# Performance work log

Hardware: AMD Instinct MI355X
Metric: run time of the kernel (lower is better)

The kernel has to match this reference:

```python
import jax, jax.numpy as jnp
import numpy as np

D = 1024      # feature_dim / vertice_dim
H = 4         # n_heads
HD = D // H   # head dim 256
DFF = 2 * D   # 2048
DV = 1024     # vertice_dim
T = 64        # frame_num
PERIOD = 30
NEG = -1e9


def setup_inputs() -> dict:
    key = jax.random.key(0)
    ks = iter(jax.random.split(key, 32))
    sc = 0.02
    def w(shape):
        return jax.random.normal(next(ks), shape, dtype=jnp.float32) * sc
    return {
        "hidden_states": jax.random.normal(next(ks), (T, DV), dtype=jnp.float32),
        "hid_w": w((D, DV)), "hid_b": w((D,)),
        "obj_w": w((D, 80)),
        "sa_in_w": w((3 * D, D)), "sa_in_b": w((3 * D,)),
        "sa_out_w": w((D, D)), "sa_out_b": w((D,)),
        "ca_in_w": w((3 * D, D)), "ca_in_b": w((3 * D,)),
        "ca_out_w": w((D, D)), "ca_out_b": w((D,)),
        "ln1_g": jnp.ones((D,), jnp.float32), "ln1_b": jnp.zeros((D,), jnp.float32),
        "ln2_g": jnp.ones((D,), jnp.float32), "ln2_b": jnp.zeros((D,), jnp.float32),
        "ln3_g": jnp.ones((D,), jnp.float32), "ln3_b": jnp.zeros((D,), jnp.float32),
        "ff1_w": w((DFF, D)), "ff1_b": w((DFF,)),
        "ff2_w": w((D, DFF)), "ff2_b": w((D,)),
        "vr_w": w((DV, D)), "vr_b": w((DV,)),
        "vm_w": w((D, DV)), "vm_b": w((D,)),
    }


def _periodic_pe():
    # sin/cos PE over one period, tiled (PeriodicPositionalEncoding)
    pos = jnp.arange(PERIOD, dtype=jnp.float32)[:, None]
    div = jnp.exp(jnp.arange(0, D, 2, dtype=jnp.float32) * (-np.log(10000.0) / D))
    pe = jnp.zeros((PERIOD, D), jnp.float32)
    pe = pe.at[:, 0::2].set(jnp.sin(pos * div)).at[:, 1::2].set(jnp.cos(pos * div))
    reps = T // PERIOD + 1
    return jnp.tile(pe, (reps, 1))[:T]  # (T, D)


def reference(hidden_states, hid_w, hid_b, obj_w,
              sa_in_w, sa_in_b, sa_out_w, sa_out_b,
              ca_in_w, ca_in_b, ca_out_w, ca_out_b,
              ln1_g, ln1_b, ln2_g, ln2_b, ln3_g, ln3_b,
              ff1_w, ff1_b, ff2_w, ff2_b, vr_w, vr_b, vm_w, vm_b):
    mem = hidden_states @ hid_w.T + hid_b          # (S=T, D)
    style = obj_w[:, 0]                             # one-hot(0) @ obj_vector
    pe = _periodic_pe()

    # ALiBi-style biased causal mask (init_biased_mask, n_head=4)
    slopes = 0.25 ** jnp.arange(1, H + 1, dtype=jnp.float32)
    idx = jnp.arange(T)
    i_, j_ = idx[:, None], idx[None, :]
    alibi = -((i_ - j_) // PERIOD).astype(jnp.float32)
    tgt_bias = jnp.where(j_ <= i_, slopes[:, None, None] * alibi[None], NEG)  # (H,T,T)
    # vocaset enc_dec_mask: frame i may only attend memory frame i
    mem_bias = jnp.where(i_ == j_, 0.0, NEG)  # (T,S)

    def mha(q_in, kv_in, in_w, in_b, out_w, out_b, bias):
        wq, wk, wv = jnp.split(in_w, 3, axis=0)
        bq, bk, bv = jnp.split(in_b, 3)
        q = (q_in @ wq.T + bq).reshape(-1, H, HD)
        k = (kv_in @ wk.T + bk).reshape(-1, H, HD)
        v = (kv_in @ wv.T + bv).reshape(-1, H, HD)
        s = jnp.einsum('qhd,khd->hqk', q, k) / np.sqrt(HD) + bias
        a = jax.nn.softmax(s, axis=-1)
        o = jnp.einsum('hqk,khd->qhd', a, v).reshape(-1, D)
        return o @ out_w.T + out_b

    def ln(x, g, b):
        m = x.mean(-1, keepdims=True)
        v = ((x - m) ** 2).mean(-1, keepdims=True)
        return (x - m) / jnp.sqrt(v + 1e-5) * g + b

    def decode(x):  # post-norm TransformerDecoderLayer (eval, dropout off)
        x = ln(x + mha(x, x, sa_in_w, sa_in_b, sa_out_w, sa_out_b, tgt_bias), ln1_g, ln1_b)
        x = ln(x + mha(x, mem, ca_in_w, ca_in_b, ca_out_w, ca_out_b, mem_bias[None]), ln2_g, ln2_b)
        h = jax.nn.relu(x @ ff1_w.T + ff1_b) @ ff2_w.T + ff2_b
        return ln(x + h, ln3_g, ln3_b)

    # independent of the zero-padded future slots, matching the growing-seq loop.
    emb0 = jnp.zeros((T, D), jnp.float32).at[0].set(style)

    def step(emb, i):
        out = decode(emb + pe)
        new_tok = (out[i] @ vr_w.T + vr_b) @ vm_w.T + vm_b + style
        return emb.at[i + 1].set(new_tok), None

    emb, _ = jax.lax.scan(step, emb0, jnp.arange(T - 1))
    # final iteration's vertice_out over the full T-length sequence
    return decode(emb + pe) @ vr_w.T + vr_b  # (T, DV)
```

## Files before the change

### kernel.cpp

```cpp
#include <hip/hip_runtime.h>
#include <math.h>

#define DIM  1024
#define SEQ  64
#define HDIM 256
#define NBLK 256

__device__ __forceinline__ float wsum(float v){
  v += __shfl_xor(v, 32, 64); v += __shfl_xor(v, 16, 64); v += __shfl_xor(v, 8, 64);
  v += __shfl_xor(v, 4, 64);  v += __shfl_xor(v, 2, 64);  v += __shfl_xor(v, 1, 64);
  return v;
}
__device__ __forceinline__ float wmax(float v){
  v = fmaxf(v, __shfl_xor(v, 32, 64)); v = fmaxf(v, __shfl_xor(v, 16, 64));
  v = fmaxf(v, __shfl_xor(v, 8, 64));  v = fmaxf(v, __shfl_xor(v, 4, 64));
  v = fmaxf(v, __shfl_xor(v, 2, 64));  v = fmaxf(v, __shfl_xor(v, 1, 64));
  return v;
}
__device__ __forceinline__ float2 breduce2(float va, float vb, float* red){
  int tid = threadIdx.x;
  va = wsum(va); vb = wsum(vb);
  if ((tid & 63) == 0){ red[(tid >> 6) * 2] = va; red[(tid >> 6) * 2 + 1] = vb; }
  __syncthreads();
  float ra = red[0] + red[2] + red[4] + red[6];
  float rb = red[1] + red[3] + red[5] + red[7];
  __syncthreads();
  return make_float2(ra, rb);
}

__device__ __forceinline__ float ldc(const float* p){
  return __hip_atomic_load(p, __ATOMIC_RELAXED, __HIP_MEMORY_SCOPE_AGENT);
}
__device__ __forceinline__ void stc(float* p, float v){
  __hip_atomic_store(p, v, __ATOMIC_RELAXED, __HIP_MEMORY_SCOPE_AGENT);
}

__device__ __forceinline__ void spin_ge(unsigned* p, unsigned ep){
  unsigned spins = 0;
  while (__hip_atomic_load(p, __ATOMIC_RELAXED, __HIP_MEMORY_SCOPE_AGENT) < ep){
    if (++spins > 4194304u){
      unsigned s2 = 0;
      while (__hip_atomic_load(p, __ATOMIC_ACQUIRE, __HIP_MEMORY_SCOPE_AGENT) < ep){
        __builtin_amdgcn_s_sleep(2);
        if (++s2 > 100000000u) break;
      }
      return;
    }
  }
}

#define SLOT_STRIDE 32
__device__ __forceinline__ void gsync(unsigned* slots, unsigned ep, int bid, int tid){
  asm volatile("s_waitcnt vmcnt(0)" ::: "memory");
  __syncthreads();
  if (tid == 0)
    __hip_atomic_store(&slots[bid * SLOT_STRIDE], ep, __ATOMIC_RELAXED, __HIP_MEMORY_SCOPE_AGENT);
  spin_ge(&slots[tid * SLOT_STRIDE], ep);
  __syncthreads();
  asm volatile("" ::: "memory");
}

__global__ void matmul_nn_1024(const float* __restrict__ A, const float* __restrict__ B,
                               float* __restrict__ Cc){
  __shared__ float As[32][33];
  __shared__ float Bs[32][33];
  int tb = blockIdx.x * 32, ta = blockIdx.y * 32;
  int tx = threadIdx.x & 31, ty = threadIdx.x >> 5;
  float acc[4] = {0.f, 0.f, 0.f, 0.f};
  for (int k0 = 0; k0 < 1024; k0 += 32){
    for (int r = ty; r < 32; r += 8) As[r][tx] = A[(size_t)(ta + r) * 1024 + k0 + tx];
    for (int r = ty; r < 32; r += 8) Bs[r][tx] = B[(size_t)(k0 + r) * 1024 + tb + tx];
    __syncthreads();
    #pragma unroll
    for (int kk = 0; kk < 32; ++kk){
      float bv = Bs[kk][tx];
      #pragma unroll
      for (int m = 0; m < 4; ++m) acc[m] = fmaf(As[ty + 8 * m][kk], bv, acc[m]);
    }
    __syncthreads();
  }
  for (int m = 0; m < 4; ++m) Cc[(size_t)(ta + ty + 8 * m) * 1024 + tb + tx] = acc[m];
}

struct CoopArgs {
  const float *hs, *hid_w, *hid_b;
  const float *sa_in_w, *sa_in_b, *sa_out_w, *sa_out_b;
  const float *ca_in_w, *ca_in_b, *ca_out_w, *ca_out_b;
  const float *ln1_g, *ln1_b, *ln2_g, *ln2_b, *ln3_g, *ln3_b;
  const float *ff1_w, *ff1_b, *ff2_w, *ff2_b;
  const float *vr_w, *vr_b, *vm_w, *vm_b, *obj_w;
  const float *Cm;
  float *pe, *emb, *kc, *vc, *mem, *vtmp, *cac, *q, *u, *hb, *w, *s;
  float *out;
  unsigned *bar;
  unsigned *flags;
};

__global__ void __launch_bounds__(256, 2) decode_loop(CoopArgs a){
  const int tid = threadIdx.x, bid = blockIdx.x;
  const int wave = tid >> 6, lane = tid & 63;
  const int gw = bid * 4 + wave;
  __shared__ float sm[2048];
  __shared__ float scp[256];
  __shared__ float red[8];
  unsigned* slots = a.bar;
  unsigned ep = 0;

  const float NLOG = -9.210340371976184f / 1024.0f;
  const float divw = __expf((float)(2 * (gw >> 1)) * NLOG);
  const int parw = gw & 1;

  {
    float pw[16];
    const float* pr = a.hid_w + (size_t)gw * DIM;
    #pragma unroll
    for (int k = 0; k < 16; ++k) pw[k] = pr[lane + 64 * k];
    float bias = a.hid_b[gw];
    for (int t = 0; t < 64; ++t){
      const float* xr = a.hs + (size_t)t * DIM;
      float acc = 0.f;
      #pragma unroll
      for (int k = 0; k < 16; ++k) acc = fmaf(pw[k], xr[lane + 64 * k], acc);
      acc = wsum(acc);
      if (lane == 0) stc(a.mem + (size_t)t * DIM + gw, acc + bias);
    }
    {
      float arg = (float)(lane % 30) * divw;
      float pev = parw ? cosf(arg) : sinf(arg);
      stc(a.pe + (size_t)lane * DIM + gw, pev);
    }
    if (bid == 0){
      for (int d = tid; d < DIM; d += 256) stc(a.emb + d, a.obj_w[(size_t)d * 80]);
    }
  }
  ++ep; gsync(slots, ep, bid, tid);

  {
    float pw[16];
    const float* pr = a.ca_in_w + (size_t)(2 * DIM + gw) * DIM;
    #pragma unroll
    for (int k = 0; k < 16; ++k) pw[k] = pr[lane + 64 * k];
    float bias = a.ca_in_b[2 * DIM + gw];
    for (int t = 0; t < 64; ++t){
      const float* xr = a.mem + (size_t)t * DIM;
      #pragma unroll
      for (int k = 0; k < 4; ++k) sm[tid + 256 * k] = ldc(xr + tid + 256 * k);
      __syncthreads();
      float acc = 0.f;
      #pragma unroll
      for (int k = 0; k < 16; ++k) acc = fmaf(pw[k], sm[lane + 64 * k], acc);
      acc = wsum(acc);
      if (lane == 0) stc(a.vtmp + (size_t)t * DIM + gw, acc + bias);
      __syncthreads();
    }
  }
  ++ep; gsync(slots, ep, bid, tid);

  {
    float pw[16];
    const float* pr = a.ca_out_w + (size_t)gw * DIM;
    #pragma unroll
    for (int k = 0; k < 16; ++k) pw[k] = pr[lane + 64 * k];
    float bias = a.ca_out_b[gw];
    for (int t = 0; t < 64; ++t){
      const float* xr = a.vtmp + (size_t)t * DIM;
      #pragma unroll
      for (int k = 0; k < 4; ++k) sm[tid + 256 * k] = ldc(xr + tid + 256 * k);
      __syncthreads();
      float acc = 0.f;
      #pragma unroll
      for (int k = 0; k < 16; ++k) acc = fmaf(pw[k], sm[lane + 64 * k], acc);
      acc = wsum(acc);
      if (lane == 0) stc(a.cac + (size_t)t * DIM + gw, acc + bias);
      __syncthreads();
    }
  }
  ++ep; gsync(slots, ep, bid, tid);

  float wq[16], wk[16], wv[16], wo[16], f1a[16], f1b[16], f2[32];
  {
    const float* pq = a.sa_in_w + (size_t)gw * DIM;
    const float* pk = a.sa_in_w + (size_t)(DIM + gw) * DIM;
    const float* pv = a.sa_in_w + (size_t)(2 * DIM + gw) * DIM;
    const float* po = a.sa_out_w + (size_t)gw * DIM;
    const float* p1a = a.ff1_w + (size_t)(2 * gw) * DIM;
    const float* p1b = a.ff1_w + (size_t)(2 * gw + 1) * DIM;
    const float* p2 = a.ff2_w + (size_t)gw * 2048;
    #pragma unroll
    for (int k = 0; k < 16; ++k){
      int d = lane + 64 * k;
      wq[k] = pq[d]; wk[k] = pk[d]; wv[k] = pv[d]; wo[k] = po[d];
      f1a[k] = p1a[d]; f1b[k] = p1b[d];
    }
    #pragma unroll
    for (int k = 0; k < 32; ++k) f2[k] = p2[lane + 64 * k];
  }
  const float b_q  = a.sa_in_b[gw];
  const float b_k  = a.sa_in_b[DIM + gw];
  const float b_v  = a.sa_in_b[2 * DIM + gw];
  const float b_o  = a.sa_out_b[gw];
  const float b_1a = a.ff1_b[2 * gw];
  const float b_1b = a.ff1_b[2 * gw + 1];
  const float b_2  = a.ff2_b[gw];
  const float b_vr = a.vr_b[gw];
  float cbv;
  {
    const float* pv = a.vm_w + (size_t)gw * DIM;
    float acc = 0.f;
    #pragma unroll
    for (int k = 0; k < 16; ++k) acc = fmaf(pv[lane + 64 * k], a.vr_b[lane + 64 * k], acc);
    cbv = wsum(acc) + a.vm_b[gw] + a.obj_w[(size_t)gw * 80];
  }

  float c0 = 0.f, c1 = 0.f, c2 = 0.f, c3 = 0.f;

  const bool is_score = (bid < 16);
  const int sc_h  = bid >> 2;
  const int sc_jg = bid & 3;
  const float sc_slope = 1.0f / (float)(4 << (2 * sc_h));

  for (int i = 0; i < SEQ; ++i){
    const float* per = a.pe + (size_t)i * DIM;

    {
      float* xs = sm;
      const float* er = a.emb + (size_t)i * DIM;
      #pragma unroll
      for (int k = 0; k < 4; ++k){
        int d = tid + 256 * k;
        xs[d] = ldc(er + d) + ldc(per + d);
      }
      __syncthreads();
      float aq = 0.f, ak = 0.f, av = 0.f;
      #pragma unroll
      for (int k = 0; k < 16; ++k){
        float x = xs[lane + 64 * k];
        aq = fmaf(wq[k], x, aq);
        ak = fmaf(wk[k], x, ak);
        av = fmaf(wv[k], x, av);
      }
      aq = wsum(aq); ak = wsum(ak); av = wsum(av);
      if (lane == 0){
        stc(a.q + gw, aq + b_q);
        stc(a.kc + (size_t)i * DIM + gw, ak + b_k);
        stc(a.vc + (size_t)i * DIM + gw, av + b_v);
      }
      __syncthreads();
    }
    ++ep; gsync(slots, ep, bid, tid);

    {
      float* xs  = sm;
      float* qsl = sm + 1024;
      float remb = ldc(a.emb + (size_t)i * DIM + gw);
      #pragma unroll
      for (int k = 0; k < 4; ++k) xs[tid + 256 * k] = ldc(a.vc + (size_t)i * DIM + tid + 256 * k);
      if (is_score) qsl[tid] = ldc(a.q + sc_h * HDIM + tid);
      __syncthreads();
      float p0 = 0.f, p1 = 0.f, p2 = 0.f, p3 = 0.f;
      #pragma unroll
      for (int k = 0; k < 4; ++k){
        p0 = fmaf(wo[k],      xs[lane + 64 * k],        p0);
        p1 = fmaf(wo[k + 4],  xs[lane + 64 * (k + 4)],  p1);
        p2 = fmaf(wo[k + 8],  xs[lane + 64 * (k + 8)],  p2);
        p3 = fmaf(wo[k + 12], xs[lane + 64 * (k + 12)], p3);
      }
      p0 = wsum(p0); p1 = wsum(p1); p2 = wsum(p2); p3 = wsum(p3);
      if (lane == i){ c0 = p0; c1 = p1; c2 = p2; c3 = p3; }
      if (is_score){
        #pragma unroll
        for (int jj = 0; jj < 4; ++jj){
          int j = sc_jg * 16 + wave * 4 + jj;
          if (j <= i){
            const float* kr = a.kc + (size_t)j * DIM + sc_h * HDIM;
            float acc = 0.f;
            #pragma unroll
            for (int m = 0; m < 4; ++m)
              acc = fmaf(qsl[m * 64 + lane], ldc(kr + m * 64 + lane), acc);
            acc = wsum(acc);
            if (lane == 0)
              stc(a.s + sc_h * 64 + j, acc * 0.0625f - sc_slope * (float)((i - j) / 30));
          }
        }
        asm volatile("s_waitcnt vmcnt(0)" ::: "memory");
        __syncthreads();
        if (tid == 0)
          __hip_atomic_store(&a.flags[bid * SLOT_STRIDE], (unsigned)(i + 1),
                             __ATOMIC_RELAXED, __HIP_MEMORY_SCOPE_AGENT);
      }
      if (tid < 16) spin_ge(&a.flags[tid * SLOT_STRIDE], (unsigned)(i + 1));
      __syncthreads();
      {
        const int h = wave;
        float sv = (lane <= i) ? ldc(a.s + h * 64 + lane) : -3.0e38f;
        float mx = wmax(sv);
        float p = (lane <= i) ? __expf(sv - mx) : 0.f;
        float sum = wsum(p);
        scp[h * 64 + lane] = p / sum;
      }
      __syncthreads();
      float t = scp[lane] * c0 + scp[64 + lane] * c1 + scp[128 + lane] * c2 + scp[192 + lane] * c3;
      t = wsum(t);
      if (lane == 0){
        stc(a.u + gw, remb + ldc(per + gw) + t + b_o);
      }
      __syncthreads();
    }
    ++ep; gsync(slots, ep, bid, tid);

    float x2v;
    {
      float* xs = sm;
      #pragma unroll
      for (int k = 0; k < 4; ++k) xs[tid + 256 * k] = ldc(a.u + tid + 256 * k);
      __syncthreads();
      float sa = 0.f, sb = 0.f;
      #pragma unroll
      for (int k = 0; k < 4; ++k){ float x = xs[tid + 256 * k]; sa += x; sb = fmaf(x, x, sb); }
      float2 r = breduce2(sa, sb, red);
      float mean = r.x * (1.f / 1024.f);
      float var = r.y * (1.f / 1024.f) - mean * mean;
      float rs = 1.f / sqrtf(var + 1e-5f);
      float tv[4];
      float ta = 0.f, tb = 0.f;
      #pragma unroll
      for (int k = 0; k < 4; ++k){
        int d = tid + 256 * k;
        float x1 = (xs[d] - mean) * rs * a.ln1_g[d] + a.ln1_b[d];
        tv[k] = x1 + ldc(a.cac + (size_t)i * DIM + d);
        ta += tv[k]; tb = fmaf(tv[k], tv[k], tb);
      }
      float2 r2 = breduce2(ta, tb, red);
      float mean2 = r2.x * (1.f / 1024.f);
      float var2 = r2.y * (1.f / 1024.f) - mean2 * mean2;
      float rs2 = 1.f / sqrtf(var2 + 1e-5f);
      #pragma unroll
      for (int k = 0; k < 4; ++k){
        int d = tid + 256 * k;
        xs[d] = (tv[k] - mean2) * rs2 * a.ln2_g[d] + a.ln2_b[d];
      }
      __syncthreads();
      x2v = xs[gw];
      float acc0 = 0.f, acc1 = 0.f;
      #pragma unroll
      for (int k = 0; k < 16; ++k){
        float x = xs[lane + 64 * k];
        acc0 = fmaf(f1a[k], x, acc0);
        acc1 = fmaf(f1b[k], x, acc1);
      }
      acc0 = wsum(acc0); acc1 = wsum(acc1);
      if (lane == 0){
        stc(a.hb + 2 * gw,     fmaxf(acc0 + b_1a, 0.f));
        stc(a.hb + 2 * gw + 1, fmaxf(acc1 + b_1b, 0.f));
      }
      __syncthreads();
    }
    ++ep; gsync(slots, ep, bid, tid);

    float vrr[16], cmr[16];
    {
      float* hsm = sm;
      #pragma unroll
      for (int k = 0; k < 8; ++k) hsm[tid + 256 * k] = ldc(a.hb + tid + 256 * k);
      const float* pr = a.vr_w + (size_t)gw * DIM;
      const float* pc = a.Cm + (size_t)gw * DIM;
      #pragma unroll
      for (int k = 0; k < 16; ++k){ vrr[k] = pr[lane + 64 * k]; cmr[k] = pc[lane + 64 * k]; }
      __syncthreads();
      float acc = 0.f;
      #pragma unroll
      for (int k = 0; k < 32; ++k) acc = fmaf(f2[k], hsm[lane + 64 * k], acc);
      acc = wsum(acc);
      if (lane == 0) stc(a.w + gw, x2v + acc + b_2);
      __syncthreads();
    }
    ++ep; gsync(slots, ep, bid, tid);

    {
      float* xs = sm;
      #pragma unroll
      for (int k = 0; k < 4; ++k) xs[tid + 256 * k] = ldc(a.w + tid + 256 * k);
      __syncthreads();
      float sa = 0.f, sb = 0.f;
      #pragma unroll
      for (int k = 0; k < 4; ++k){ float x = xs[tid + 256 * k]; sa += x; sb = fmaf(x, x, sb); }
      float2 r = breduce2(sa, sb, red);
      float mean = r.x * (1.f / 1024.f);
      float var = r.y * (1.f / 1024.f) - mean * mean;
      float rs = 1.f / sqrtf(var + 1e-5f);
      float ov[4];
      #pragma unroll
      for (int k = 0; k < 4; ++k){
        int d = tid + 256 * k;
        ov[k] = (xs[d] - mean) * rs * a.ln3_g[d] + a.ln3_b[d];
      }
      __syncthreads();
      #pragma unroll
      for (int k = 0; k < 4; ++k) xs[tid + 256 * k] = ov[k];
      __syncthreads();
      {
        float ar = 0.f, ac = 0.f;
        #pragma unroll
        for (int k = 0; k < 16; ++k){
          float x = xs[lane + 64 * k];
          ar = fmaf(vrr[k], x, ar);
          ac = fmaf(cmr[k], x, ac);
        }
        ar = wsum(ar); ac = wsum(ac);
        if (lane == 0){
          a.out[(size_t)i * DIM + gw] = ar + b_vr;
          if (i < SEQ - 1) stc(a.emb + (size_t)(i + 1) * DIM + gw, ac + cbv);
        }
      }
      __syncthreads();
    }
    ++ep; gsync(slots, ep, bid, tid);
  }
}

extern "C" void kernel_launch(void* const* d_in, const int* in_sizes, int n_in,
                              void* d_out, int out_size, void* d_ws, size_t ws_size,
                              hipStream_t stream){
  const float* hs       = (const float*)d_in[0];
  const float* hid_w    = (const float*)d_in[1];
  const float* hid_b    = (const float*)d_in[2];
  const float* obj_w    = (const float*)d_in[3];
  const float* sa_in_w  = (const float*)d_in[4];
  const float* sa_in_b  = (const float*)d_in[5];
  const float* sa_out_w = (const float*)d_in[6];
  const float* sa_out_b = (const float*)d_in[7];
  const float* ca_in_w  = (const float*)d_in[8];
  const float* ca_in_b  = (const float*)d_in[9];
  const float* ca_out_w = (const float*)d_in[10];
  const float* ca_out_b = (const float*)d_in[11];
  const float* ln1_g    = (const float*)d_in[12];
  const float* ln1_b    = (const float*)d_in[13];
  const float* ln2_g    = (const float*)d_in[14];
  const float* ln2_b    = (const float*)d_in[15];
  const float* ln3_g    = (const float*)d_in[16];
  const float* ln3_b    = (const float*)d_in[17];
  const float* ff1_w    = (const float*)d_in[18];
  const float* ff1_b    = (const float*)d_in[19];
  const float* ff2_w    = (const float*)d_in[20];
  const float* ff2_b    = (const float*)d_in[21];
  const float* vr_w     = (const float*)d_in[22];
  const float* vr_b     = (const float*)d_in[23];
  const float* vm_w     = (const float*)d_in[24];
  const float* vm_b     = (const float*)d_in[25];

  float* ws = (float*)d_ws;
  float* pe   = ws;
  float* emb  = ws + 65536;
  float* kc   = ws + 131072;
  float* vc   = ws + 196608;
  float* mem  = ws + 262144;
  float* vtmp = ws + 327680;
  float* cac  = ws + 393216;
  float* Cm   = ws + 458752;
  float* q    = ws + 1507328;
  float* u    = ws + 1508352;
  float* hb   = ws + 1509376;
  float* wv   = ws + 1511424;
  float* sbuf = ws + 1512448;
  unsigned* bar   = (unsigned*)(ws + 1513472);
  unsigned* flags = bar + 256 * SLOT_STRIDE;

  hipMemsetAsync((void*)bar, 0, (256 + 16) * SLOT_STRIDE * 4, stream);

  matmul_nn_1024<<<dim3(32, 32), 256, 0, stream>>>(vm_w, vr_w, Cm);

  CoopArgs A;
  A.hs = hs; A.hid_w = hid_w; A.hid_b = hid_b;
  A.sa_in_w = sa_in_w; A.sa_in_b = sa_in_b; A.sa_out_w = sa_out_w; A.sa_out_b = sa_out_b;
  A.ca_in_w = ca_in_w; A.ca_in_b = ca_in_b; A.ca_out_w = ca_out_w; A.ca_out_b = ca_out_b;
  A.ln1_g = ln1_g; A.ln1_b = ln1_b; A.ln2_g = ln2_g; A.ln2_b = ln2_b; A.ln3_g = ln3_g; A.ln3_b = ln3_b;
  A.ff1_w = ff1_w; A.ff1_b = ff1_b; A.ff2_w = ff2_w; A.ff2_b = ff2_b;
  A.vr_w = vr_w; A.vr_b = vr_b; A.vm_w = vm_w; A.vm_b = vm_b; A.obj_w = obj_w;
  A.Cm = Cm;
  A.pe = pe; A.emb = emb; A.kc = kc; A.vc = vc; A.mem = mem; A.vtmp = vtmp; A.cac = cac;
  A.q = q; A.u = u; A.hb = hb; A.w = wv; A.s = sbuf;
  A.out = (float*)d_out;
  A.bar = bar; A.flags = flags;

  void* params[1] = { &A };
  hipError_t e = hipLaunchCooperativeKernel((void*)decode_loop, dim3(NBLK), dim3(256), params, 0, stream);
  if (e != hipSuccess){
    decode_loop<<<dim3(NBLK), dim3(256), 0, stream>>>(A);
  }
}
```

Measured before the change: 2.176 ms.

## Replace per-stage grid barriers with epoch-tagged data lines polled directly

Drops the five grid-wide barriers per decode step. Each producer now writes its result together with an epoch tag into a 128-byte line using a cache-bypassing dwordx4 store, and consumers spin on those lines until the tag reaches the current step, so data and synchronization travel in one transaction. Positional encoding is recomputed in registers instead of read from a buffer, and the score exchange goes through tagged lines instead of a separate flag array. This removes barrier round-trips on the serial critical path, at the cost of heavier polling traffic (1024 lines per stage) and reliance on the ordering of 16-byte stores.

Result: slower. 2.803 ms (+28.8%).

```diff
diff --git a/kernel.cpp b/kernel.cpp
--- a/kernel.cpp
+++ b/kernel.cpp
@@ -5,6 +5,9 @@
 #define SEQ  64
 #define HDIM 256
 #define NBLK 256
+#define SLOT_STRIDE 32
+
+typedef float f4 __attribute__((ext_vector_type(4)));
 
 __device__ __forceinline__ float wsum(float v){
   v += __shfl_xor(v, 32, 64); v += __shfl_xor(v, 16, 64); v += __shfl_xor(v, 8, 64);
@@ -35,6 +38,46 @@
   __hip_atomic_store(p, v, __ATOMIC_RELAXED, __HIP_MEMORY_SCOPE_AGENT);
 }
 
+__device__ __forceinline__ void st_line(float* p, float x, float y, float z, float w){
+  f4 v; v.x = x; v.y = y; v.z = z; v.w = w;
+  asm volatile("global_store_dwordx4 %0, %1, off sc0 sc1" :: "v"(p), "v"(v) : "memory");
+}
+__device__ __forceinline__ f4 ld_line(const float* p){
+  f4 r;
+  asm volatile("global_load_dwordx4 %0, %1, off sc0 sc1\n\ts_waitcnt vmcnt(0)"
+               : "=v"(r) : "v"(p) : "memory");
+  return r;
+}
+__device__ __forceinline__ void poll4(const float* base, int tid, float tgt,
+                                      f4& r0, f4& r1, f4& r2, f4& r3){
+  const float* p0 = base + (size_t)tid * 32;
+  const float* p1 = base + (size_t)(tid + 256) * 32;
+  const float* p2 = base + (size_t)(tid + 512) * 32;
+  const float* p3 = base + (size_t)(tid + 768) * 32;
+  unsigned spins = 0;
+  for (;;){
+    asm volatile(
+      "global_load_dwordx4 %0, %4, off sc0 sc1\n\t"
+      "global_load_dwordx4 %1, %5, off sc0 sc1\n\t"
+      "global_load_dwordx4 %2, %6, off sc0 sc1\n\t"
+      "global_load_dwordx4 %3, %7, off sc0 sc1\n\t"
+      "s_waitcnt vmcnt(0)"
+      : "=&v"(r0), "=&v"(r1), "=&v"(r2), "=&v"(r3)
+      : "v"(p0), "v"(p1), "v"(p2), "v"(p3)
+      : "memory");
+    if (r0.w >= tgt && r1.w >= tgt && r2.w >= tgt && r3.w >= tgt) return;
+    if (++spins > 100000000u) return;
+  }
+}
+__device__ __forceinline__ f4 poll1(const float* p, float tgt){
+  unsigned spins = 0;
+  for (;;){
+    f4 r = ld_line(p);
+    if (r.w >= tgt) return r;
+    if (++spins > 100000000u) return r;
+  }
+}
+
 __device__ __forceinline__ void spin_ge(unsigned* p, unsigned ep){
   unsigned spins = 0;
   while (__hip_atomic_load(p, __ATOMIC_RELAXED, __HIP_MEMORY_SCOPE_AGENT) < ep){
@@ -48,8 +91,6 @@
     }
   }
 }
-
-#define SLOT_STRIDE 32
 __device__ __forceinline__ void gsync(unsigned* slots, unsigned ep, int bid, int tid){
   asm volatile("s_waitcnt vmcnt(0)" ::: "memory");
   __syncthreads();
@@ -90,25 +131,31 @@
   const float *ff1_w, *ff1_b, *ff2_w, *ff2_b;
   const float *vr_w, *vr_b, *vm_w, *vm_b, *obj_w;
   const float *Cm;
-  float *pe, *emb, *kc, *vc, *mem, *vtmp, *cac, *q, *u, *hb, *w, *s;
+  float *mem, *vtmp, *cac, *kc;
+  float *lS1, *lU, *lH, *lW, *lE, *lSC;
   float *out;
   unsigned *bar;
-  unsigned *flags;
 };
 
 __global__ void __launch_bounds__(256, 2) decode_loop(CoopArgs a){
   const int tid = threadIdx.x, bid = blockIdx.x;
   const int wave = tid >> 6, lane = tid & 63;
   const int gw = bid * 4 + wave;
-  __shared__ float sm[2048];
+  __shared__ float smA[2048];
+  __shared__ float smB[1024];
+  __shared__ float smC[1024];
   __shared__ float scp[256];
   __shared__ float red[8];
-  unsigned* slots = a.bar;
   unsigned ep = 0;
 
   const float NLOG = -9.210340371976184f / 1024.0f;
-  const float divw = __expf((float)(2 * (gw >> 1)) * NLOG);
-  const int parw = gw & 1;
+  float div4[4]; int par4[4];
+  #pragma unroll
+  for (int k = 0; k < 4; ++k){
+    int d = tid + 256 * k;
+    div4[k] = __expf((float)(2 * (d >> 1)) * NLOG);
+    par4[k] = d & 1;
+  }
 
   {
     float pw[16];
@@ -124,16 +171,8 @@
       acc = wsum(acc);
       if (lane == 0) stc(a.mem + (size_t)t * DIM + gw, acc + bias);
     }
-    {
-      float arg = (float)(lane % 30) * divw;
-      float pev = parw ? cosf(arg) : sinf(arg);
-      stc(a.pe + (size_t)lane * DIM + gw, pev);
-    }
-    if (bid == 0){
-      for (int d = tid; d < DIM; d += 256) stc(a.emb + d, a.obj_w[(size_t)d * 80]);
-    }
-  }
-  ++ep; gsync(slots, ep, bid, tid);
+  }
+  ++ep; gsync(a.bar, ep, bid, tid);
 
   {
     float pw[16];
@@ -144,17 +183,17 @@
     for (int t = 0; t < 64; ++t){
       const float* xr = a.mem + (size_t)t * DIM;
       #pragma unroll
-      for (int k = 0; k < 4; ++k) sm[tid + 256 * k] = ldc(xr + tid + 256 * k);
+      for (int k = 0; k < 4; ++k) smA[tid + 256 * k] = ldc(xr + tid + 256 * k);
       __syncthreads();
       float acc = 0.f;
       #pragma unroll
-      for (int k = 0; k < 16; ++k) acc = fmaf(pw[k], sm[lane + 64 * k], acc);
+      for (int k = 0; k < 16; ++k) acc = fmaf(pw[k], smA[lane + 64 * k], acc);
       acc = wsum(acc);
       if (lane == 0) stc(a.vtmp + (size_t)t * DIM + gw, acc + bias);
       __syncthreads();
     }
   }
-  ++ep; gsync(slots, ep, bid, tid);
+  ++ep; gsync(a.bar, ep, bid, tid);
 
   {
     float pw[16];
@@ -165,17 +204,17 @@
     for (int t = 0; t < 64; ++t){
       const float* xr = a.vtmp + (size_t)t * DIM;
       #pragma unroll
-      for (int k = 0; k < 4; ++k) sm[tid + 256 * k] = ldc(xr + tid + 256 * k);
+      for (int k = 0; k < 4; ++k) smA[tid + 256 * k] = ldc(xr + tid + 256 * k);
       __syncthreads();
       float acc = 0.f;
       #pragma unroll
-      for (int k = 0; k < 16; ++k) acc = fmaf(pw[k], sm[lane + 64 * k], acc);
+      for (int k = 0; k < 16; ++k) acc = fmaf(pw[k], smA[lane + 64 * k], acc);
       acc = wsum(acc);
       if (lane == 0) stc(a.cac + (size_t)t * DIM + gw, acc + bias);
       __syncthreads();
     }
   }
-  ++ep; gsync(slots, ep, bid, tid);
+  ++ep; gsync(a.bar, ep, bid, tid);
 
   float wq[16], wk[16], wv[16], wo[16], f1a[16], f1b[16], f2[32];
   {
@@ -217,57 +256,71 @@
   const bool is_score = (bid < 16);
   const int sc_h  = bid >> 2;
   const int sc_jg = bid & 3;
+  const int swid  = bid * 4 + wave;
   const float sc_slope = 1.0f / (float)(4 << (2 * sc_h));
 
   for (int i = 0; i < SEQ; ++i){
-    const float* per = a.pe + (size_t)i * DIM;
+    const float posf = (float)(i % 30);
+    const float epf  = (float)(i + 1);
+    float remb;
 
     {
-      float* xs = sm;
-      const float* er = a.emb + (size_t)i * DIM;
-      #pragma unroll
-      for (int k = 0; k < 4; ++k){
-        int d = tid + 256 * k;
-        xs[d] = ldc(er + d) + ldc(per + d);
-      }
-      __syncthreads();
+      if (i == 0){
+        #pragma unroll
+        for (int k = 0; k < 4; ++k){
+          int d = tid + 256 * k;
+          float arg = posf * div4[k];
+          float pe = par4[k] ? cosf(arg) : sinf(arg);
+          smA[d] = a.obj_w[(size_t)d * 80] + pe;
+        }
+      } else {
+        f4 r0, r1, r2, r3;
+        poll4(a.lE, tid, (float)i, r0, r1, r2, r3);
+        float ev[4] = {r0.x, r1.x, r2.x, r3.x};
+        #pragma unroll
+        for (int k = 0; k < 4; ++k){
+          int d = tid + 256 * k;
+          float arg = posf * div4[k];
+          float pe = par4[k] ? cosf(arg) : sinf(arg);
+          smA[d] = ev[k] + pe;
+        }
+      }
+      __syncthreads();
+      remb = smA[gw];
       float aq = 0.f, ak = 0.f, av = 0.f;
       #pragma unroll
       for (int k = 0; k < 16; ++k){
-        float x = xs[lane + 64 * k];
+        float x = smA[lane + 64 * k];
         aq = fmaf(wq[k], x, aq);
         ak = fmaf(wk[k], x, ak);
         av = fmaf(wv[k], x, av);
       }
       aq = wsum(aq); ak = wsum(ak); av = wsum(av);
       if (lane == 0){
-        stc(a.q + gw, aq + b_q);
         stc(a.kc + (size_t)i * DIM + gw, ak + b_k);
-        stc(a.vc + (size_t)i * DIM + gw, av + b_v);
-      }
-      __syncthreads();
-    }
-    ++ep; gsync(slots, ep, bid, tid);
+        asm volatile("s_waitcnt vmcnt(0)" ::: "memory");
+        st_line(a.lS1 + (size_t)gw * 32, aq + b_q, ak + b_k, av + b_v, epf);
+      }
+    }
 
     {
-      float* xs  = sm;
-      float* qsl = sm + 1024;
-      float remb = ldc(a.emb + (size_t)i * DIM + gw);
-      #pragma unroll
-      for (int k = 0; k < 4; ++k) xs[tid + 256 * k] = ldc(a.vc + (size_t)i * DIM + tid + 256 * k);
-      if (is_score) qsl[tid] = ldc(a.q + sc_h * HDIM + tid);
+      f4 r0, r1, r2, r3;
+      poll4(a.lS1, tid, epf, r0, r1, r2, r3);
+      smB[tid] = r0.z; smB[tid + 256] = r1.z; smB[tid + 512] = r2.z; smB[tid + 768] = r3.z;
+      smC[tid] = r0.x; smC[tid + 256] = r1.x; smC[tid + 512] = r2.x; smC[tid + 768] = r3.x;
       __syncthreads();
       float p0 = 0.f, p1 = 0.f, p2 = 0.f, p3 = 0.f;
       #pragma unroll
       for (int k = 0; k < 4; ++k){
-        p0 = fmaf(wo[k],      xs[lane + 64 * k],        p0);
-        p1 = fmaf(wo[k + 4],  xs[lane + 64 * (k + 4)],  p1);
-        p2 = fmaf(wo[k + 8],  xs[lane + 64 * (k + 8)],  p2);
-        p3 = fmaf(wo[k + 12], xs[lane + 64 * (k + 12)], p3);
+        p0 = fmaf(wo[k],      smB[lane + 64 * k],        p0);
+        p1 = fmaf(wo[k + 4],  smB[lane + 64 * (k + 4)],  p1);
+        p2 = fmaf(wo[k + 8],  smB[lane + 64 * (k + 8)],  p2);
+        p3 = fmaf(wo[k + 12], smB[lane + 64 * (k + 12)], p3);
       }
       p0 = wsum(p0); p1 = wsum(p1); p2 = wsum(p2); p3 = wsum(p3);
       if (lane == i){ c0 = p0; c1 = p1; c2 = p2; c3 = p3; }
       if (is_score){
+        float sj[4];
         #pragma unroll
         for (int jj = 0; jj < 4; ++jj){
           int j = sc_jg * 16 + wave * 4 + jj;
@@ -276,23 +329,28 @@
             float acc = 0.f;
             #pragma unroll
             for (int m = 0; m < 4; ++m)
-              acc = fmaf(qsl[m * 64 + lane], ldc(kr + m * 64 + lane), acc);
+              acc = fmaf(smC[sc_h * HDIM + m * 64 + lane], ldc(kr + m * 64 + lane), acc);
             acc = wsum(acc);
-            if (lane == 0)
-              stc(a.s + sc_h * 64 + j, acc * 0.0625f - sc_slope * (float)((i - j) / 30));
-          }
+            sj[jj] = acc * 0.0625f - sc_slope * (float)((i - j) / 30);
+          } else sj[jj] = 0.f;
         }
-        asm volatile("s_waitcnt vmcnt(0)" ::: "memory");
-        __syncthreads();
-        if (tid == 0)
-          __hip_atomic_store(&a.flags[bid * SLOT_STRIDE], (unsigned)(i + 1),
-                             __ATOMIC_RELAXED, __HIP_MEMORY_SCOPE_AGENT);
-      }
-      if (tid < 16) spin_ge(&a.flags[tid * SLOT_STRIDE], (unsigned)(i + 1));
+        if (lane == 0){
+          st_line(a.lSC + (size_t)(swid * 2) * 32,     sj[0], sj[1], 0.f, epf);
+          st_line(a.lSC + (size_t)(swid * 2 + 1) * 32, sj[2], sj[3], 0.f, epf);
+        }
+      }
+      if (tid < 128){
+        f4 r = poll1(a.lSC + (size_t)tid * 32, epf);
+        int sw = tid >> 1, half = tid & 1;
+        int sb = sw >> 2, wv2 = sw & 3;
+        int h = sb >> 2, jg = sb & 3;
+        int j0 = jg * 16 + wv2 * 4 + half * 2;
+        scp[h * 64 + j0] = r.x; scp[h * 64 + j0 + 1] = r.y;
+      }
       __syncthreads();
       {
         const int h = wave;
-        float sv = (lane <= i) ? ldc(a.s + h * 64 + lane) : -3.0e38f;
+        float sv = (lane <= i) ? scp[h * 64 + lane] : -3.0e38f;
         float mx = wmax(sv);
         float p = (lane <= i) ? __expf(sv - mx) : 0.f;
         float sum = wsum(p);
@@ -301,120 +359,112 @@
       __syncthreads();
       float t = scp[lane] * c0 + scp[64 + lane] * c1 + scp[128 + lane] * c2 + scp[192 + lane] * c3;
       t = wsum(t);
-      if (lane == 0){
-        stc(a.u + gw, remb + ldc(per + gw) + t + b_o);
-      }
-      __syncthreads();
-    }
-    ++ep; gsync(slots, ep, bid, tid);
+      if (lane == 0) st_line(a.lU + (size_t)gw * 32, remb + t + b_o, 0.f, 0.f, epf);
+    }
 
     float x2v;
     {
-      float* xs = sm;
-      #pragma unroll
-      for (int k = 0; k < 4; ++k) xs[tid + 256 * k] = ldc(a.u + tid + 256 * k);
+      float cr[4];
+      #pragma unroll
+      for (int k = 0; k < 4; ++k) cr[k] = ldc(a.cac + (size_t)i * DIM + tid + 256 * k);
+      f4 r0, r1, r2, r3;
+      poll4(a.lU, tid, epf, r0, r1, r2, r3);
+      smA[tid] = r0.x; smA[tid + 256] = r1.x; smA[tid + 512] = r2.x; smA[tid + 768] = r3.x;
       __syncthreads();
       float sa = 0.f, sb = 0.f;
       #pragma unroll
-      for (int k = 0; k < 4; ++k){ float x = xs[tid + 256 * k]; sa += x; sb = fmaf(x, x, sb); }
+      for (int k = 0; k < 4; ++k){ float x = smA[tid + 256 * k]; sa += x; sb = fmaf(x, x, sb); }
       float2 r = breduce2(sa, sb, red);
       float mean = r.x * (1.f / 1024.f);
-      float var = r.y * (1.f / 1024.f) - mean * mean;
+      float var  = r.y * (1.f / 1024.f) - mean * mean;
       float rs = 1.f / sqrtf(var + 1e-5f);
       float tv[4];
       float ta = 0.f, tb = 0.f;
       #pragma unroll
       for (int k = 0; k < 4; ++k){
         int d = tid + 256 * k;
-        float x1 = (xs[d] - mean) * rs * a.ln1_g[d] + a.ln1_b[d];
-        tv[k] = x1 + ldc(a.cac + (size_t)i * DIM + d);
+        float x1 = (smA[d] - mean) * rs * a.ln1_g[d] + a.ln1_b[d];
+        tv[k] = x1 + cr[k];
         ta += tv[k]; tb = fmaf(tv[k], tv[k], tb);
       }
-      float2 r2 = breduce2(ta, tb, red);
-      float mean2 = r2.x * (1.f / 1024.f);
-      float var2 = r2.y * (1.f / 1024.f) - mean2 * mean2;
+      float2 r2v = breduce2(ta, tb, red);
+      float mean2 = r2v.x * (1.f / 1024.f);
+      float var2  = r2v.y * (1.f / 1024.f) - mean2 * mean2;
       float rs2 = 1.f / sqrtf(var2 + 1e-5f);
       #pragma unroll
       for (int k = 0; k < 4; ++k){
         int d = tid + 256 * k;
-        xs[d] = (tv[k] - mean2) * rs2 * a.ln2_g[d] + a.ln2_b[d];
-      }
-      __syncthreads();
-      x2v = xs[gw];
+        smA[d] = (tv[k] - mean2) * rs2 * a.ln2_g[d] + a.ln2_b[d];
+      }
+      __syncthreads();
+      x2v = smA[gw];
       float acc0 = 0.f, acc1 = 0.f;
       #pragma unroll
       for (int k = 0; k < 16; ++k){
-        float x = xs[lane + 64 * k];
+        float x = smA[lane + 64 * k];
         acc0 = fmaf(f1a[k], x, acc0);
         acc1 = fmaf(f1b[k], x, acc1);
       }
       acc0 = wsum(acc0); acc1 = wsum(acc1);
-      if (lane == 0){
-        stc(a.hb + 2 * gw,     fmaxf(acc0 + b_1a, 0.f));
-        stc(a.hb + 2 * gw + 1, fmaxf(acc1 + b_1b, 0.f));
-      }
-      __syncthreads();
-    }
-    ++ep; gsync(slots, ep, bid, tid);
+      if (lane == 0)
+        st_line(a.lH + (size_t)gw * 32, fmaxf(acc0 + b_1a, 0.f), fmaxf(acc1 + b_1b, 0.f), 0.f, epf);
+    }
 
     float vrr[16], cmr[16];
     {
-      float* hsm = sm;
-      #pragma unroll
-      for (int k = 0; k < 8; ++k) hsm[tid + 256 * k] = ldc(a.hb + tid + 256 * k);
       const float* pr = a.vr_w + (size_t)gw * DIM;
       const float* pc = a.Cm + (size_t)gw * DIM;
       #pragma unroll
       for (int k = 0; k < 16; ++k){ vrr[k] = pr[lane + 64 * k]; cmr[k] = pc[lane + 64 * k]; }
+      f4 r0, r1, r2, r3;
+      poll4(a.lH, tid, epf, r0, r1, r2, r3);
+      smA[2 * tid] = r0.x;           smA[2 * tid + 1] = r0.y;
+      smA[2 * (tid + 256)] = r1.x;   smA[2 * (tid + 256) + 1] = r1.y;
+      smA[2 * (tid + 512)] = r2.x;   smA[2 * (tid + 512) + 1] = r2.y;
+      smA[2 * (tid + 768)] = r3.x;   smA[2 * (tid + 768) + 1] = r3.y;
       __syncthreads();
       float acc = 0.f;
       #pragma unroll
-      for (int k = 0; k < 32; ++k) acc = fmaf(f2[k], hsm[lane + 64 * k], acc);
+      for (int k = 0; k < 32; ++k) acc = fmaf(f2[k], smA[lane + 64 * k], acc);
       acc = wsum(acc);
-      if (lane == 0) stc(a.w + gw, x2v + acc + b_2);
-      __syncthreads();
-    }
-    ++ep; gsync(slots, ep, bid, tid);
+      if (lane == 0) st_line(a.lW + (size_t)gw * 32, x2v + acc + b_2, 0.f, 0.f, epf);
+    }
 
     {
-      float* xs = sm;
-      #pragma unroll
-      for (int k = 0; k < 4; ++k) xs[tid + 256 * k] = ldc(a.w + tid + 256 * k);
+      f4 r0, r1, r2, r3;
+      poll4(a.lW, tid, epf, r0, r1, r2, r3);
+      smA[tid] = r0.x; smA[tid + 256] = r1.x; smA[tid + 512] = r2.x; smA[tid + 768] = r3.x;
       __syncthreads();
       float sa = 0.f, sb = 0.f;
       #pragma unroll
-      for (int k = 0; k < 4; ++k){ float x = xs[tid + 256 * k]; sa += x; sb = fmaf(x, x, sb); }
+      for (int k = 0; k < 4; ++k){ float x = smA[tid + 256 * k]; sa += x; sb = fmaf(x, x, sb); }
       float2 r = breduce2(sa, sb, red);
       float mean = r.x * (1.f / 1024.f);
-      float var = r.y * (1.f / 1024.f) - mean * mean;
+      float var  = r.y * (1.f / 1024.f) - mean * mean;
       float rs = 1.f / sqrtf(var + 1e-5f);
       float ov[4];
       #pragma unroll
       for (int k = 0; k < 4; ++k){
         int d = tid + 256 * k;
-        ov[k] = (xs[d] - mean) * rs * a.ln3_g[d] + a.ln3_b[d];
-      }
-      __syncthreads();
-      #pragma unroll
-      for (int k = 0; k < 4; ++k) xs[tid + 256 * k] = ov[k];
-      __syncthreads();
-      {
-        float ar = 0.f, ac = 0.f;
-        #pragma unroll
-        for (int k = 0; k < 16; ++k){
-          float x = xs[lane + 64 * k];
-          ar = fmaf(vrr[k], x, ar);
-          ac = fmaf(cmr[k], x, ac);
-        }
-        ar = wsum(ar); ac = wsum(ac);
-        if (lane == 0){
-          a.out[(size_t)i * DIM + gw] = ar + b_vr;
-          if (i < SEQ - 1) stc(a.emb + (size_t)(i + 1) * DIM + gw, ac + cbv);
-        }
-      }
-      __syncthreads();
-    }
-    ++ep; gsync(slots, ep, bid, tid);
+        ov[k] = (smA[d] - mean) * rs * a.ln3_g[d] + a.ln3_b[d];
+      }
+      __syncthreads();
+      #pragma unroll
+      for (int k = 0; k < 4; ++k) smA[tid + 256 * k] = ov[k];
+      __syncthreads();
+      float ar = 0.f, ac = 0.f;
+      #pragma unroll
+      for (int k = 0; k < 16; ++k){
+        float x = smA[lane + 64 * k];
+        ar = fmaf(vrr[k], x, ar);
+        ac = fmaf(cmr[k], x, ac);
+      }
+      ar = wsum(ar); ac = wsum(ac);
+      if (lane == 0){
+        a.out[(size_t)i * DIM + gw] = ar + b_vr;
+        st_line(a.lE + (size_t)gw * 32, ac + cbv, 0.f, 0.f, epf);
+      }
+    }
   }
 }
 
@@ -449,23 +499,20 @@
   const float* vm_b     = (const float*)d_in[25];
 
   float* ws = (float*)d_ws;
-  float* pe   = ws;
-  float* emb  = ws + 65536;
-  float* kc   = ws + 131072;
-  float* vc   = ws + 196608;
-  float* mem  = ws + 262144;
-  float* vtmp = ws + 327680;
-  float* cac  = ws + 393216;
-  float* Cm   = ws + 458752;
-  float* q    = ws + 1507328;
-  float* u    = ws + 1508352;
-  float* hb   = ws + 1509376;
-  float* wv   = ws + 1511424;
-  float* sbuf = ws + 1512448;
-  unsigned* bar   = (unsigned*)(ws + 1513472);
-  unsigned* flags = bar + 256 * SLOT_STRIDE;
-
-  hipMemsetAsync((void*)bar, 0, (256 + 16) * SLOT_STRIDE * 4, stream);
+  float* mem  = ws;
+  float* vtmp = ws + 65536;
+  float* cac  = ws + 131072;
+  float* kc   = ws + 196608;
+  float* Cm   = ws + 262144;
+  float* lS1  = ws + 1310720;
+  float* lU   = ws + 1343488;
+  float* lH   = ws + 1376256;
+  float* lW   = ws + 1409024;
+  float* lE   = ws + 1441792;
+  float* lSC  = ws + 1474560;
+  unsigned* bar = (unsigned*)(ws + 1478656);
+
+  hipMemsetAsync((void*)lS1, 0, (size_t)(167936 + 8192) * 4, stream);
 
   matmul_nn_1024<<<dim3(32, 32), 256, 0, stream>>>(vm_w, vr_w, Cm);
 
@@ -477,10 +524,10 @@
   A.ff1_w = ff1_w; A.ff1_b = ff1_b; A.ff2_w = ff2_w; A.ff2_b = ff2_b;
   A.vr_w = vr_w; A.vr_b = vr_b; A.vm_w = vm_w; A.vm_b = vm_b; A.obj_w = obj_w;
   A.Cm = Cm;
-  A.pe = pe; A.emb = emb; A.kc = kc; A.vc = vc; A.mem = mem; A.vtmp = vtmp; A.cac = cac;
-  A.q = q; A.u = u; A.hb = hb; A.w = wv; A.s = sbuf;
+  A.mem = mem; A.vtmp = vtmp; A.cac = cac; A.kc = kc;
+  A.lS1 = lS1; A.lU = lU; A.lH = lH; A.lW = lW; A.lE = lE; A.lSC = lSC;
   A.out = (float*)d_out;
-  A.bar = bar; A.flags = flags;
+  A.bar = bar;
 
   void* params[1] = { &A };
   hipError_t e = hipLaunchCooperativeKernel((void*)decode_loop, dim3(NBLK), dim3(256), params, 0, stream);
```
